# Optimization experiments

Measured on AMD Instinct MI355X. Metric: run time of the kernel, lower is better.

## Reference

```python
import jax, jax.numpy as jnp
import numpy as np

N_NODES = 100000


def gcn_conv(x, edge_index, W, b, n):
    """PyG-style GCNConv: h = D^-1/2 (A + I) D^-1/2 (x W) + b."""
    h = x @ W  # [n, out]
    loops = jnp.arange(n, dtype=edge_index.dtype)
    src = jnp.concatenate([edge_index[0], loops])
    dst = jnp.concatenate([edge_index[1], loops])
    deg = jax.ops.segment_sum(jnp.ones_like(dst, dtype=h.dtype), dst, num_segments=n)
    dinv = jnp.where(deg > 0, jax.lax.rsqrt(deg), 0.0)
    norm = dinv[src] * dinv[dst]  # [E+n]
    msg = h[src] * norm[:, None]
    out = jax.ops.segment_sum(msg, dst, num_segments=n)
    return out + b


def setup_inputs() -> dict:
    key = jax.random.key(0)
    ks = jax.random.split(key, 12)
    n, f, hid, c, e = N_NODES, 128, 16, 32, 3200000
    x = jax.random.normal(ks[0], (n, f), dtype=jnp.float32)
    edge_index_pos = jax.random.randint(ks[1], (2, e), 0, n, dtype=jnp.int32)
    edge_index_neg = jax.random.randint(ks[2], (2, e), 0, n, dtype=jnp.int32)
    def glorot(k, fi, fo):
        lim = np.sqrt(6.0 / (fi + fo)).astype(np.float32)
        return jax.random.uniform(k, (fi, fo), minval=-lim, maxval=lim, dtype=jnp.float32)
    return {
        "x": x,
        "edge_index_pos": edge_index_pos,
        "edge_index_neg": edge_index_neg,
        "W1p": glorot(ks[3], f, hid), "b1p": jnp.zeros((hid,), jnp.float32),
        "W1n": glorot(ks[4], f, hid), "b1n": jnp.zeros((hid,), jnp.float32),
        "W2p": glorot(ks[5], hid, c), "b2p": jnp.zeros((c,), jnp.float32),
        "W2n": glorot(ks[6], hid, c), "b2n": jnp.zeros((c,), jnp.float32),
    }


def reference(x, edge_index_pos, edge_index_neg, W1p, b1p, W1n, b1n, W2p, b2p, W2n, b2n):
    n = x.shape[0]
    # layer 1: relu(pos) - relu(neg)
    h = (jax.nn.relu(gcn_conv(x, edge_index_pos, W1p, b1p, n))
         - jax.nn.relu(gcn_conv(x, edge_index_neg, W1n, b1n, n)))
    # dropout is identity in eval mode (training=False)
    h = (jax.nn.relu(gcn_conv(h, edge_index_pos, W2p, b2p, n))
         - jax.nn.relu(gcn_conv(h, edge_index_neg, W2n, b2n, n)))
    return jax.nn.log_softmax(h, axis=1)
```

## Files before the change

### kernel.cpp

```cpp
#include <hip/hip_runtime.h>
#include <hip/hip_fp16.h>


#define BSHIFT 8
#define BSZ 256
#define MAX_NBK 512
#define FILL_CAP 13056
#define SORT_CAP 12032

__device__ __forceinline__ int chunk_of_block(int bid, int NCH) {
  return (NCH % 8 == 0) ? (bid % 8) * (NCH / 8) + bid / 8 : bid;
}


__global__ __launch_bounds__(256) void bucket_count2(
    const int* __restrict__ eP, const int* __restrict__ eN,
    int E, int CH, int NCH, int NBK, int* __restrict__ ccP, int* __restrict__ ccN) {
  __shared__ int cnt[MAX_NBK];
  const int* dsts = (blockIdx.y ? eN : eP) + E;
  int* cc = blockIdx.y ? ccN : ccP;
  const int c = chunk_of_block(blockIdx.x, NCH);
  for (int i = threadIdx.x; i < NBK; i += 256) cnt[i] = 0;
  __syncthreads();
  int base = c * CH, end = min(E, base + CH);
  for (int idx = base + threadIdx.x; idx < end; idx += 256)
    atomicAdd(&cnt[dsts[idx] >> BSHIFT], 1);
  __syncthreads();
  for (int i = threadIdx.x; i < NBK; i += 256)
    cc[(size_t)c * NBK + i] = cnt[i];
}

__global__ __launch_bounds__(512) void col_scan2(
    int* __restrict__ ccP, int* __restrict__ ccN, int NCH, int NBK,
    int* __restrict__ totP, int* __restrict__ totN) {
  __shared__ int s[512];
  int* cc = blockIdx.y ? ccN : ccP;
  int* tot = blockIdx.y ? totN : totP;
  int b = blockIdx.x, t = threadIdx.x;
  int v = (t < NCH) ? cc[(size_t)t * NBK + b] : 0;
  s[t] = v;
  for (int off = 1; off < 512; off <<= 1) {
    __syncthreads();
    int a = (t >= off) ? s[t - off] : 0;
    __syncthreads();
    s[t] += a;
  }
  __syncthreads();
  if (t < NCH) cc[(size_t)t * NBK + b] = s[t] - v;
  if (t == 511) tot[b] = s[511];
}

__global__ __launch_bounds__(512) void base_scan(
    const int* __restrict__ totP, const int* __restrict__ totN, int NBK,
    int* __restrict__ baseP, int* __restrict__ baseN,
    int* __restrict__ rowP, int* __restrict__ rowN, int n, int E) {
  __shared__ int sp[512], sn[512];
  __shared__ int carryP, carryN;
  int t = threadIdx.x;
  if (t == 0) { carryP = 0; carryN = 0; }
  __syncthreads();
  for (int tile = 0; tile < NBK; tile += 512) {
    int idx = tile + t;
    int vp = (idx < NBK) ? totP[idx] : 0;
    int vn = (idx < NBK) ? totN[idx] : 0;
    sp[t] = vp; sn[t] = vn;
    for (int off = 1; off < 512; off <<= 1) {
      __syncthreads();
      int ap = (t >= off) ? sp[t - off] : 0;
      int an = (t >= off) ? sn[t - off] : 0;
      __syncthreads();
      sp[t] += ap; sn[t] += an;
    }
    __syncthreads();
    if (idx < NBK) {
      baseP[idx] = carryP + sp[t] - vp;
      baseN[idx] = carryN + sn[t] - vn;
    }
    __syncthreads();
    if (t == 0) { carryP += sp[511]; carryN += sn[511]; }
    __syncthreads();
  }
  if (t == 0) {
    baseP[NBK] = E; baseN[NBK] = E;
    rowP[n] = E; rowN[n] = E;
  }
}

__global__ __launch_bounds__(512) void bucket_fill3(
    const int* __restrict__ eP, const int* __restrict__ eN,
    int E, int CH, int NCH, int NBK,
    const int* __restrict__ ccP, const int* __restrict__ ccN,
    const int* __restrict__ totP, const int* __restrict__ totN,
    const int* __restrict__ basP, const int* __restrict__ basN,
    unsigned* __restrict__ prP, unsigned* __restrict__ prN) {
  __shared__ unsigned obuf[FILL_CAP];
  __shared__ int chofs[MAX_NBK], hist[MAX_NBK], lofs[MAX_NBK], cur[MAX_NBK];
  __shared__ int s[512];
  const int* edges = blockIdx.y ? eN : eP;
  const int* cc = blockIdx.y ? ccN : ccP;
  const int* tot = blockIdx.y ? totN : totP;
  const int* bas = blockIdx.y ? basN : basP;
  unsigned* pairs = blockIdx.y ? prN : prP;
  const int c = chunk_of_block(blockIdx.x, NCH);
  const int t = threadIdx.x;

  int h = 0;
  if (t < NBK) {
    int o0 = cc[(size_t)c * NBK + t];
    int o1 = (c + 1 < NCH) ? cc[(size_t)(c + 1) * NBK + t] : tot[t];
    chofs[t] = o0;
    h = o1 - o0;
    hist[t] = h;
  }
  s[t] = h;
  for (int off = 1; off < 512; off <<= 1) {
    __syncthreads();
    int a = (t >= off) ? s[t - off] : 0;
    __syncthreads();
    s[t] += a;
  }
  __syncthreads();
  if (t < NBK) { lofs[t] = s[t] - hist[t]; cur[t] = s[t] - hist[t]; }
  __syncthreads();

  int base = c * CH, end = min(E, base + CH);
  for (int idx = base + t; idx < end; idx += 512) {
    int sv = edges[idx], d = edges[E + idx];
    int b = d >> BSHIFT;
    int pos = atomicAdd(&cur[b], 1);
    obuf[pos] = (unsigned)sv | ((unsigned)(d & (BSZ - 1)) << 24);
  }
  __syncthreads();

  if (t < NBK) {
    int cnt = hist[t], lo = lofs[t];
    unsigned* dst = pairs + (size_t)bas[t] + chofs[t];
    for (int j = 0; j < cnt; ++j) dst[j] = obuf[lo + j];
  }
}

__global__ __launch_bounds__(256) void tile_sort3(
    const unsigned* __restrict__ prP, const unsigned* __restrict__ prN,
    const int* __restrict__ basP, const int* __restrict__ basN, int n,
    float* __restrict__ dinvP, float* __restrict__ dinvN,
    int* __restrict__ rowP, int* __restrict__ rowN,
    unsigned* __restrict__ srcsP, unsigned* __restrict__ srcsN) {
  __shared__ unsigned obuf[SORT_CAP];
  __shared__ int hist[BSZ];
  __shared__ int scn[BSZ];
  __shared__ int cur[BSZ];
  const unsigned* pairs = blockIdx.y ? prN : prP;
  const int* base = blockIdx.y ? basN : basP;
  float* dinv = blockIdx.y ? dinvN : dinvP;
  int* rowoff = blockIdx.y ? rowN : rowP;
  unsigned* srcs = blockIdx.y ? srcsN : srcsP;
  const int b = blockIdx.x, t = threadIdx.x;
  const int s0 = base[b], s1 = base[b + 1], cnt = s1 - s0;
  hist[t] = 0;
  __syncthreads();
  for (int i = s0 + t; i < s1; i += 256)
    atomicAdd(&hist[pairs[i] >> 24], 1);
  __syncthreads();
  scn[t] = hist[t];
  __syncthreads();
  for (int off = 1; off < BSZ; off <<= 1) {
    int v = (t >= off) ? scn[t - off] : 0;
    __syncthreads();
    scn[t] += v;
    __syncthreads();
  }
  {
    int excl = scn[t] - hist[t];
    cur[t] = excl;
    int node = b * BSZ + t;
    if (node < n) {
      rowoff[node] = s0 + excl;
      dinv[node] = rsqrtf(1.0f + (float)hist[t]);
    }
  }
  __syncthreads();
  if (cnt <= SORT_CAP) {
    for (int i = s0 + t; i < s1; i += 256) {
      unsigned p = pairs[i];
      int pos = atomicAdd(&cur[p >> 24], 1);
      obuf[pos] = p & 0xFFFFFFu;
    }
    __syncthreads();
    for (int i = t; i < cnt; i += 256) srcs[s0 + i] = obuf[i];
  } else {
    for (int i = s0 + t; i < s1; i += 256) {
      unsigned p = pairs[i];
      int pos = atomicAdd(&cur[p >> 24], 1);
      srcs[s0 + pos] = p & 0xFFFFFFu;
    }
  }
}

__global__ __launch_bounds__(256) void xw1_kernel(
    const float* __restrict__ x, const float* __restrict__ Wp, const float* __restrict__ Wn,
    const float* __restrict__ dinvP, const float* __restrict__ dinvN,
    __half* __restrict__ hp, __half* __restrict__ hn, int n)
{
  __shared__ float xs[16 * 132];
  __shared__ float wp[128 * 16], wn[128 * 16];
  const int tid = threadIdx.x;
  const int rowBase = blockIdx.x * 16;

  for (int idx = tid; idx < 512; idx += 256) {
    ((float4*)wp)[idx] = ((const float4*)Wp)[idx];
    ((float4*)wn)[idx] = ((const float4*)Wn)[idx];
  }
  const int nrows = min(16, n - rowBase);
  for (int idx = tid; idx < nrows * 32; idx += 256) {
    int r = idx >> 5, c4 = idx & 31;
    float4 v = ((const float4*)(x + (size_t)(rowBase + r) * 128))[c4];
    *(float4*)(xs + r * 132 + c4 * 4) = v;
  }
  __syncthreads();

  const int r = tid >> 4, c = tid & 15;
  const int i = rowBase + r;
  if (i < n) {
    float ap = 0.f, an = 0.f;
    #pragma unroll
    for (int k = 0; k < 128; ++k) {
      float xv = xs[r * 132 + k];
      ap += xv * wp[k * 16 + c];
      an += xv * wn[k * 16 + c];
    }
    hp[(size_t)i * 16 + c] = __float2half(ap * dinvP[i]);
    hn[(size_t)i * 16 + c] = __float2half(an * dinvN[i]);
  }
}

__device__ __forceinline__ float seg_sum(
    const unsigned* __restrict__ srcs, int e, int e1,
    const __half* __restrict__ tab, int lane, float acc)
{
  float acc2 = 0.f;
  for (; e + 16 <= e1; e += 16) {
    unsigned a[16];
    #pragma unroll
    for (int j = 0; j < 16; ++j) a[j] = srcs[e + j];
    float v[16];
    #pragma unroll
    for (int j = 0; j < 16; ++j) v[j] = __half2float(tab[(size_t)a[j] * 16 + lane]);
    acc  += ((v[0] + v[1]) + (v[2] + v[3])) + ((v[4] + v[5]) + (v[6] + v[7]));
    acc2 += ((v[8] + v[9]) + (v[10] + v[11])) + ((v[12] + v[13]) + (v[14] + v[15]));
  }
  for (; e + 4 <= e1; e += 4) {
    unsigned a0 = srcs[e], a1 = srcs[e+1], a2 = srcs[e+2], a3 = srcs[e+3];
    float v0 = __half2float(tab[(size_t)a0 * 16 + lane]);
    float v1 = __half2float(tab[(size_t)a1 * 16 + lane]);
    float v2 = __half2float(tab[(size_t)a2 * 16 + lane]);
    float v3 = __half2float(tab[(size_t)a3 * 16 + lane]);
    acc += (v0 + v1) + (v2 + v3);
  }
  for (; e < e1; ++e) acc += __half2float(tab[(size_t)srcs[e] * 16 + lane]);
  return acc + acc2;
}

__global__ __launch_bounds__(256) void agg_split(
    const unsigned* __restrict__ srcP, const int* __restrict__ rowP,
    const unsigned* __restrict__ srcN, const int* __restrict__ rowN,
    const __half* __restrict__ inP, const __half* __restrict__ inN,
    const float* __restrict__ dinvP, const float* __restrict__ dinvN,
    float* __restrict__ tmpP, float* __restrict__ tmpN, int n)
{
  const int gb = blockIdx.x;
  const int xcd = gb & 7;
  const int sign = xcd >> 2;
  const int nblk = (gb >> 3) * 4 + (xcd & 3);
  const int lane = threadIdx.x & 15, grp = threadIdx.x >> 4;
  const int i = nblk * 16 + grp;
  if (i >= n) return;

  const unsigned* srcs = sign ? srcN : srcP;
  const int* row = sign ? rowN : rowP;
  const __half* tab = sign ? inN : inP;
  const float* dinv = sign ? dinvN : dinvP;
  float* tmp = sign ? tmpN : tmpP;

  float acc = __half2float(tab[(size_t)i * 16 + lane]);
  acc = seg_sum(srcs, row[i], row[i + 1], tab, lane, acc);
  tmp[(size_t)i * 16 + lane] = dinv[i] * acc;
}

__global__ __launch_bounds__(256) void combine1(
    const float* __restrict__ tmpP, const float* __restrict__ tmpN,
    const float* __restrict__ bp, const float* __restrict__ bn,
    const float* __restrict__ dinvP, const float* __restrict__ dinvN,
    __half* __restrict__ Gp, __half* __restrict__ Gn, long long total)
{
  long long j = (long long)blockIdx.x * 256 + threadIdx.x;
  if (j >= total) return;
  int i = (int)(j >> 4), lane = (int)(j & 15);
  float ap = bp[lane] + tmpP[j];
  float an = bn[lane] + tmpN[j];
  float h = fmaxf(ap, 0.f) - fmaxf(an, 0.f);
  Gp[j] = __float2half(h * dinvP[i]);
  Gn[j] = __float2half(h * dinvN[i]);
}

__global__ __launch_bounds__(256) void final2(
    const float* __restrict__ Up, const float* __restrict__ Un,
    const float* __restrict__ W2p, const float* __restrict__ W2n,
    const float* __restrict__ b2p, const float* __restrict__ b2n,
    float* __restrict__ out, int n)
{
  __shared__ float wp[16 * 32], wn[16 * 32];
  for (int i = threadIdx.x; i < 512; i += 256) { wp[i] = W2p[i]; wn[i] = W2n[i]; }
  __syncthreads();

  const int tid = threadIdx.x;
  const int lane = tid & 15, grp = tid >> 4;
  const int i = blockIdx.x * 16 + grp;
  if (i >= n) return;

  float tp = Up[(size_t)i * 16 + lane];
  float tn = Un[(size_t)i * 16 + lane];

  float ap0 = b2p[lane], ap1 = b2p[lane + 16];
  float an0 = b2n[lane], an1 = b2n[lane + 16];
  #pragma unroll
  for (int k = 0; k < 16; ++k) {
    float tpk = __shfl(tp, k, 16);
    float tnk = __shfl(tn, k, 16);
    ap0 += tpk * wp[k * 32 + lane];
    ap1 += tpk * wp[k * 32 + lane + 16];
    an0 += tnk * wn[k * 32 + lane];
    an1 += tnk * wn[k * 32 + lane + 16];
  }
  float v0 = fmaxf(ap0, 0.f) - fmaxf(an0, 0.f);
  float v1 = fmaxf(ap1, 0.f) - fmaxf(an1, 0.f);
  float m = fmaxf(v0, v1);
  #pragma unroll
  for (int off = 8; off > 0; off >>= 1) m = fmaxf(m, __shfl_xor(m, off, 16));
  float s = __expf(v0 - m) + __expf(v1 - m);
  #pragma unroll
  for (int off = 8; off > 0; off >>= 1) s += __shfl_xor(s, off, 16);
  float ls = __logf(s);
  out[(size_t)i * 32 + lane] = v0 - m - ls;
  out[(size_t)i * 32 + lane + 16] = v1 - m - ls;
}

extern "C" void kernel_launch(void* const* d_in, const int* in_sizes, int n_in,
                              void* d_out, int out_size, void* d_ws, size_t ws_size,
                              hipStream_t stream) {
  const float* x   = (const float*)d_in[0];
  const int*   eP  = (const int*)d_in[1];
  const int*   eN  = (const int*)d_in[2];
  const float* W1p = (const float*)d_in[3];
  const float* b1p = (const float*)d_in[4];
  const float* W1n = (const float*)d_in[5];
  const float* b1n = (const float*)d_in[6];
  const float* W2p = (const float*)d_in[7];
  const float* b2p = (const float*)d_in[8];
  const float* W2n = (const float*)d_in[9];
  const float* b2n = (const float*)d_in[10];
  float* out = (float*)d_out;

  const int HID = in_sizes[4];
  const int F   = in_sizes[3] / HID;
  const int n   = in_sizes[0] / F;
  const int E   = in_sizes[1] / 2;
  (void)out_size; (void)n_in; (void)ws_size;

  const int NBK = (n + BSZ - 1) >> BSHIFT;
  const int CH  = (((E + 255) / 256) + 255) & ~255;
  const int NCH = (E + CH - 1) / CH;

  char* p = (char*)d_ws;
  auto alloc = [&](size_t bytes) { char* r = p; p += (bytes + 255) & ~(size_t)255; return r; };

  int*      ccP   = (int*)alloc((size_t)NCH * NBK * 4);
  int*      ccN   = (int*)alloc((size_t)NCH * NBK * 4);
  int*      totP  = (int*)alloc((size_t)NBK * 4);
  int*      totN  = (int*)alloc((size_t)NBK * 4);
  int*      basP  = (int*)alloc((size_t)(NBK + 1) * 4);
  int*      basN  = (int*)alloc((size_t)(NBK + 1) * 4);
  unsigned* prP   = (unsigned*)alloc((size_t)E * 4);
  unsigned* prN   = (unsigned*)alloc((size_t)E * 4);
  unsigned* srcP  = (unsigned*)alloc((size_t)E * 4);
  unsigned* srcN  = (unsigned*)alloc((size_t)E * 4);
  int*      rowP  = (int*)alloc((size_t)(n + 1) * 4);
  int*      rowN  = (int*)alloc((size_t)(n + 1) * 4);
  float*    dinvP = (float*)alloc((size_t)n * 4);
  float*    dinvN = (float*)alloc((size_t)n * 4);
  __half*   hsP   = (__half*)alloc((size_t)n * 16 * 2);
  __half*   hsN   = (__half*)alloc((size_t)n * 16 * 2);
  __half*   Gp    = (__half*)alloc((size_t)n * 16 * 2);
  __half*   Gn    = (__half*)alloc((size_t)n * 16 * 2);
  float*    tmpP  = (float*)alloc((size_t)n * 16 * 4);
  float*    tmpN  = (float*)alloc((size_t)n * 16 * 4);

  hipLaunchKernelGGL(bucket_count2, dim3(NCH, 2), dim3(256), 0, stream,
                     eP, eN, E, CH, NCH, NBK, ccP, ccN);
  hipLaunchKernelGGL(col_scan2, dim3(NBK, 2), dim3(512), 0, stream,
                     ccP, ccN, NCH, NBK, totP, totN);
  hipLaunchKernelGGL(base_scan, dim3(1), dim3(512), 0, stream,
                     totP, totN, NBK, basP, basN, rowP, rowN, n, E);
  hipLaunchKernelGGL(bucket_fill3, dim3(NCH, 2), dim3(512), 0, stream,
                     eP, eN, E, CH, NCH, NBK, ccP, ccN, totP, totN,
                     basP, basN, prP, prN);
  hipLaunchKernelGGL(tile_sort3, dim3(NBK, 2), dim3(256), 0, stream,
                     prP, prN, basP, basN, n, dinvP, dinvN, rowP, rowN, srcP, srcN);

  const int NB   = (n + 15) / 16;
  const int NBS  = ((NB + 3) / 4) * 4;
  const int GRID = NBS * 2;

  hipLaunchKernelGGL(xw1_kernel, dim3(NB), dim3(256), 0, stream,
                     x, W1p, W1n, dinvP, dinvN, hsP, hsN, n);
  hipLaunchKernelGGL(agg_split, dim3(GRID), dim3(256), 0, stream,
                     srcP, rowP, srcN, rowN, hsP, hsN, dinvP, dinvN, tmpP, tmpN, n);
  hipLaunchKernelGGL(combine1, dim3((int)(((long long)n * 16 + 255) / 256)), dim3(256), 0, stream,
                     tmpP, tmpN, b1p, b1n, dinvP, dinvN, Gp, Gn, (long long)n * 16);

  hipLaunchKernelGGL(agg_split, dim3(GRID), dim3(256), 0, stream,
                     srcP, rowP, srcN, rowN, Gp, Gn, dinvP, dinvN, tmpP, tmpN, n);
  hipLaunchKernelGGL(final2, dim3(NB), dim3(256), 0, stream,
                     tmpP, tmpN, W2p, W2n, b2p, b2n, out, n);
}
```

Baseline: 246.1 us.

## Vectorize aggregation gathers to 4 halfs per lane with fma_mix accumulation

The aggregation kernel now assigns 4 threads per node instead of 16, and each thread gathers an 8-byte chunk of 4 half values per neighbor rather than one 2-byte half. The values are accumulated with inline v_fma_mix_f32 instructions that convert and add in one step, and the output is written as a float4. This cuts the number of gather instructions and conversions per edge and lets each thread handle more edges in flight. The trade-off is fewer threads per node and more serial work per thread on high-degree rows, plus non-portable inline assembly.

```diff
diff --git a/kernel.cpp b/kernel.cpp
--- a/kernel.cpp
+++ b/kernel.cpp
@@ -233,31 +233,50 @@
   }
 }
 
-__device__ __forceinline__ float seg_sum(
+__device__ __forceinline__ void fma_mix2(float& aLo, float& aHi, unsigned h2, float one) {
+  asm("v_fma_mix_f32 %0, %2, %3, %0 op_sel:[0,0,0] op_sel_hi:[1,0,0]\n\t"
+      "v_fma_mix_f32 %1, %2, %3, %1 op_sel:[1,0,0] op_sel_hi:[1,0,0]"
+      : "+v"(aLo), "+v"(aHi)
+      : "v"(h2), "v"(one));
+}
+
+__device__ __forceinline__ void seg_sum4(
     const unsigned* __restrict__ srcs, int e, int e1,
-    const __half* __restrict__ tab, int lane, float acc)
+    const __half* __restrict__ tab, int lane4, float one,
+    float& f0, float& f1, float& f2, float& f3)
 {
-  float acc2 = 0.f;
-  for (; e + 16 <= e1; e += 16) {
-    unsigned a[16];
+  float g0 = 0.f, g1 = 0.f, g2 = 0.f, g3 = 0.f;
+  for (; e + 8 <= e1; e += 8) {
+    unsigned a[8];
     #pragma unroll
-    for (int j = 0; j < 16; ++j) a[j] = srcs[e + j];
-    float v[16];
+    for (int j = 0; j < 8; ++j) a[j] = srcs[e + j];
+    uint2 v[8];
     #pragma unroll
-    for (int j = 0; j < 16; ++j) v[j] = __half2float(tab[(size_t)a[j] * 16 + lane]);
-    acc  += ((v[0] + v[1]) + (v[2] + v[3])) + ((v[4] + v[5]) + (v[6] + v[7]));
-    acc2 += ((v[8] + v[9]) + (v[10] + v[11])) + ((v[12] + v[13]) + (v[14] + v[15]));
-  }
-  for (; e + 4 <= e1; e += 4) {
-    unsigned a0 = srcs[e], a1 = srcs[e+1], a2 = srcs[e+2], a3 = srcs[e+3];
-    float v0 = __half2float(tab[(size_t)a0 * 16 + lane]);
-    float v1 = __half2float(tab[(size_t)a1 * 16 + lane]);
-    float v2 = __half2float(tab[(size_t)a2 * 16 + lane]);
-    float v3 = __half2float(tab[(size_t)a3 * 16 + lane]);
-    acc += (v0 + v1) + (v2 + v3);
-  }
-  for (; e < e1; ++e) acc += __half2float(tab[(size_t)srcs[e] * 16 + lane]);
-  return acc + acc2;
+    for (int j = 0; j < 8; ++j)
+      v[j] = *(const uint2*)(tab + (size_t)a[j] * 16 + lane4 * 4);
+    #pragma unroll
+    for (int j = 0; j < 8; j += 2) {
+      fma_mix2(f0, f1, v[j].x, one);
+      fma_mix2(f2, f3, v[j].y, one);
+      fma_mix2(g0, g1, v[j + 1].x, one);
+      fma_mix2(g2, g3, v[j + 1].y, one);
+    }
+  }
+  for (; e + 2 <= e1; e += 2) {
+    unsigned a0 = srcs[e], a1 = srcs[e + 1];
+    uint2 v0 = *(const uint2*)(tab + (size_t)a0 * 16 + lane4 * 4);
+    uint2 v1 = *(const uint2*)(tab + (size_t)a1 * 16 + lane4 * 4);
+    fma_mix2(f0, f1, v0.x, one);
+    fma_mix2(f2, f3, v0.y, one);
+    fma_mix2(g0, g1, v1.x, one);
+    fma_mix2(g2, g3, v1.y, one);
+  }
+  if (e < e1) {
+    uint2 v = *(const uint2*)(tab + (size_t)srcs[e] * 16 + lane4 * 4);
+    fma_mix2(f0, f1, v.x, one);
+    fma_mix2(f2, f3, v.y, one);
+  }
+  f0 += g0; f1 += g1; f2 += g2; f3 += g3;
 }
 
 __global__ __launch_bounds__(256) void agg_split(
@@ -271,8 +290,8 @@
   const int xcd = gb & 7;
   const int sign = xcd >> 2;
   const int nblk = (gb >> 3) * 4 + (xcd & 3);
-  const int lane = threadIdx.x & 15, grp = threadIdx.x >> 4;
-  const int i = nblk * 16 + grp;
+  const int lane4 = threadIdx.x & 3, grp = threadIdx.x >> 2;
+  const int i = nblk * 64 + grp;
   if (i >= n) return;
 
   const unsigned* srcs = sign ? srcN : srcP;
@@ -281,9 +300,16 @@
   const float* dinv = sign ? dinvN : dinvP;
   float* tmp = sign ? tmpN : tmpP;
 
-  float acc = __half2float(tab[(size_t)i * 16 + lane]);
-  acc = seg_sum(srcs, row[i], row[i + 1], tab, lane, acc);
-  tmp[(size_t)i * 16 + lane] = dinv[i] * acc;
+  const float one = 1.0f;
+  float f0 = 0.f, f1 = 0.f, f2 = 0.f, f3 = 0.f;
+  uint2 self = *(const uint2*)(tab + (size_t)i * 16 + lane4 * 4);
+  fma_mix2(f0, f1, self.x, one);
+  fma_mix2(f2, f3, self.y, one);
+  seg_sum4(srcs, row[i], row[i + 1], tab, lane4, one, f0, f1, f2, f3);
+  const float d = dinv[i];
+  float4 o;
+  o.x = f0 * d; o.y = f1 * d; o.z = f2 * d; o.w = f3 * d;
+  *(float4*)(tmp + (size_t)i * 16 + lane4 * 4) = o;
 }
 
 __global__ __launch_bounds__(256) void combine1(
@@ -406,11 +432,12 @@
   hipLaunchKernelGGL(tile_sort3, dim3(NBK, 2), dim3(256), 0, stream,
                      prP, prN, basP, basN, n, dinvP, dinvN, rowP, rowN, srcP, srcN);
 
-  const int NB   = (n + 15) / 16;
-  const int NBS  = ((NB + 3) / 4) * 4;
+  const int NB16 = (n + 15) / 16;
+  const int NB64 = (n + 63) / 64;
+  const int NBS  = ((NB64 + 3) / 4) * 4;
   const int GRID = NBS * 2;
 
-  hipLaunchKernelGGL(xw1_kernel, dim3(NB), dim3(256), 0, stream,
+  hipLaunchKernelGGL(xw1_kernel, dim3(NB16), dim3(256), 0, stream,
                      x, W1p, W1n, dinvP, dinvN, hsP, hsN, n);
   hipLaunchKernelGGL(agg_split, dim3(GRID), dim3(256), 0, stream,
                      srcP, rowP, srcN, rowN, hsP, hsN, dinvP, dinvN, tmpP, tmpN, n);
@@ -419,6 +446,6 @@
 
   hipLaunchKernelGGL(agg_split, dim3(GRID), dim3(256), 0, stream,
                      srcP, rowP, srcN, rowN, Gp, Gn, dinvP, dinvN, tmpP, tmpN, n);
-  hipLaunchKernelGGL(final2, dim3(NB), dim3(256), 0, stream,
+  hipLaunchKernelGGL(final2, dim3(NB16), dim3(256), 0, stream,
                      tmpP, tmpN, W2p, W2n, b2p, b2n, out, n);
 }
```

Measured after the change: 241.1 us. 2.0% less time.
